# Performance work log

Measured on AMD Instinct MI355X. Metric: run time of the kernel, lower is better.

## Reference

```python
import jax, jax.numpy as jnp
import numpy as np

N = 50000      # nodes
E = 800000     # edges per sampled adjacency
F_IN = 128     # input features
H = 256        # hidden
C = 112        # classes (ogbn-proteins)
L = 8          # num_layers
EPS = 1e-5     # BatchNorm eps


def setup_inputs() -> dict:
    key = jax.random.key(0)
    ks = jax.random.split(key, 8)
    x = jax.random.normal(ks[0], (N, F_IN), dtype=jnp.float32)
    edge1 = jax.random.randint(ks[1], (2, E), 0, N)
    edge2 = jax.random.randint(ks[2], (2, E), 0, N)
    in_W = jax.random.normal(ks[3], (F_IN, H), dtype=jnp.float32) * 0.05
    in_b = jnp.zeros((H,), jnp.float32)
    convW = jax.random.normal(ks[4], (L, H, H), dtype=jnp.float32) * 0.05
    convB = jnp.zeros((L, H), jnp.float32)
    bn_gamma = jnp.ones((L, H), jnp.float32)
    bn_beta = jnp.zeros((L, H), jnp.float32)
    out_W = jax.random.normal(ks[5], (H, C), dtype=jnp.float32) * 0.05
    out_b = jnp.zeros((C,), jnp.float32)
    layer_w = jax.random.normal(ks[6], (L,), dtype=jnp.float32)
    return dict(x=x, edge1=edge1, edge2=edge2, in_W=in_W, in_b=in_b,
                convW=convW, convB=convB, bn_gamma=bn_gamma, bn_beta=bn_beta,
                out_W=out_W, out_b=out_b, layer_w=layer_w)


def _gcn_norm(edge_index):
    # GCNConv default: add self-loops, sym-normalize D^{-1/2} A_hat D^{-1/2}.
    loops = jnp.arange(N)
    row = jnp.concatenate([edge_index[0], loops])  # source
    col = jnp.concatenate([edge_index[1], loops])  # target
    deg = jax.ops.segment_sum(jnp.ones_like(row, jnp.float32), col, num_segments=N)
    dinv = jnp.where(deg > 0, jax.lax.rsqrt(deg), 0.0)
    return row, col, dinv[row] * dinv[col]


def reference(x, edge1, edge2, in_W, in_b, convW, convB, bn_gamma, bn_beta,
              out_W, out_b, layer_w):
    adj1 = _gcn_norm(edge1)
    adj2 = _gcn_norm(edge2)
    h = x @ in_W + in_b                                  # input_fc: [N, H]
    w = jax.nn.softmax(layer_w)                          # residual layer weights
    acc = jnp.zeros_like(h)
    for i in range(L):
        row, col, norm = adj1 if i < L // 2 else adj2
        t = h @ convW[i] + convB[i]                      # GCNConv linear
        msg = t[row] * norm[:, None]                     # gather + scale  [E+N, H]
        h = jax.ops.segment_sum(msg, col, num_segments=N)  # scatter-add SpMM
        mu = h.mean(axis=0)                              # BatchNorm1d (batch stats)
        var = h.var(axis=0)
        h = (h - mu) * jax.lax.rsqrt(var + EPS) * bn_gamma[i] + bn_beta[i]
        h = jax.nn.relu(h)                               # dropout is identity in eval
        acc = acc + w[i] * h                             # weighted residual sum
    out = acc @ out_W + out_b                            # out_fc: [N, C]
    return jax.nn.log_softmax(out, axis=1)
```

## Files before the change

### kernel.cpp

```cpp
#include <hip/hip_runtime.h>
#include <math.h>

#define NN 50000
#define HH 256
#define FIN 128
#define CC 112
#define LL 8
#define EE 800000
#define EPSB 1e-5f
#define NGRP 8
#define NPG (NN / NGRP)
#define SLW 32
#define NSL (HH / SLW)
#define BCAP 110000

typedef unsigned short u16;
typedef unsigned int u32;
typedef __attribute__((ext_vector_type(8))) short bf16x8;
typedef __attribute__((ext_vector_type(4))) float f32x4;

__device__ __forceinline__ u16 f2bf(float f) {
    u32 u = __float_as_uint(f);
    u32 r = (u + 0x7FFFu + ((u >> 16) & 1u)) >> 16;
    return (u16)r;
}
__device__ __forceinline__ float bflo(u32 u) { return __uint_as_float(u << 16); }
__device__ __forceinline__ float bfhi(u32 u) { return __uint_as_float(u & 0xFFFF0000u); }
__device__ __forceinline__ float bf1(u16 u) { return __uint_as_float(((u32)u) << 16); }

__device__ __forceinline__ void gload16(const u16* g, u16* l) {
    __builtin_amdgcn_global_load_lds(
        (const __attribute__((address_space(1))) void*)g,
        (__attribute__((address_space(3))) void*)l, 16, 0, 0);
}

__global__ __launch_bounds__(256) void k_part(const int* __restrict__ ed1,
                                              const int* __restrict__ ed2,
                                              int* __restrict__ bcnt,
                                              u32* __restrict__ bucket) {
    __shared__ int hist[16], base[16], cnt2[16];
    const int t = threadIdx.x;
    if (t < 16) { hist[t] = 0; cnt2[t] = 0; }
    __syncthreads();
    const int e0 = blockIdx.x * 2048;
    int myb[8]; u32 myp[8];
#pragma unroll
    for (int k = 0; k < 8; ++k) {
        int e = e0 + k * 256 + t;
        myb[k] = -1;
        if (e < 2 * EE) {
            const int* ed = (e < EE) ? ed1 : ed2;
            int ee = (e < EE) ? e : e - EE;
            int c = ed[ee + EE];
            int r = ed[ee];
            int b = ((e >= EE) ? 8 : 0) | (c / NPG);
            myb[k] = b;
            myp[k] = ((u32)c << 16) | (u32)r;
            atomicAdd(&hist[b], 1);
        }
    }
    __syncthreads();
    if (t < 16) base[t] = atomicAdd(&bcnt[t], hist[t]);
    __syncthreads();
#pragma unroll
    for (int k = 0; k < 8; ++k) {
        if (myb[k] >= 0) {
            int off = atomicAdd(&cnt2[myb[k]], 1);
            bucket[(size_t)myb[k] * BCAP + base[myb[k]] + off] = myp[k];
        }
    }
}

__global__ __launch_bounds__(256) void k_fillB(const u32* __restrict__ bucket,
                                               const int* __restrict__ bcnt,
                                               int* __restrict__ cur,
                                               u16* __restrict__ src1p,
                                               u16* __restrict__ src2p) {
    const int b = blockIdx.x & 15;
    const int n = bcnt[b];
    u16* sp = (b < 8) ? src1p : src2p;
    int* cu = (b < 8) ? cur : cur + NN;
    const u32* bk = bucket + (size_t)b * BCAP;
    const int stride = (gridDim.x >> 4) * 256;
    for (int i = (blockIdx.x >> 4) * 256 + threadIdx.x; i < n; i += stride) {
        u32 p = bk[i];
        int c = p >> 16;
        int r = p & 0xFFFFu;
        int pos = atomicAdd(&cu[c], 1);
        sp[(c << 6) + pos] = (u16)r;
    }
}

__global__ void k_dinv2(const int* __restrict__ deg, float* __restrict__ dinv1,
                        float* __restrict__ dinv2, int n) {
    int v = blockIdx.x * blockDim.x + threadIdx.x;
    if (v >= 2 * n) return;
    float* d = (v < n) ? dinv1 : dinv2;
    int vv = (v < n) ? v : v - n;
    d[vv] = rsqrtf((float)(deg[v] + 1));
}

__global__ void k_wt(const float* __restrict__ W, u16* __restrict__ Wt, int K, int N) {
    __shared__ u16 sm[32][33];
    const float* Wl = W + (size_t)blockIdx.z * K * N;
    u16* Wtl = Wt + (size_t)blockIdx.z * K * N;
    int k0 = blockIdx.y * 32, n0 = blockIdx.x * 32;
    int tx = threadIdx.x, ty = threadIdx.y;
#pragma unroll
    for (int r = 0; r < 32; r += 8)
        sm[ty + r][tx] = f2bf(Wl[(size_t)(k0 + ty + r) * N + n0 + tx]);
    __syncthreads();
#pragma unroll
    for (int r = 0; r < 32; r += 8)
        Wtl[(size_t)(n0 + ty + r) * K + k0 + tx] = sm[tx][ty + r];
}

__global__ void k_outwt(const float* __restrict__ outW, const float* __restrict__ outb,
                        u16* __restrict__ outWt, float* __restrict__ obb) {
    int idx = blockIdx.x * 256 + threadIdx.x;
    if (idx >= 128 * 256) return;
    int n = idx >> 8, k = idx & 255;
    float v = (n < CC) ? outW[(size_t)k * CC + n] : 0.f;
    outWt[(size_t)n * HH + k] = f2bf(v);
    if (idx < 128) obb[idx] = (idx < CC) ? outb[idx] : 0.f;
}

__global__ void k_xcast(const float* __restrict__ x, u16* __restrict__ xb, int n4) {
    int i = blockIdx.x * blockDim.x + threadIdx.x;
    if (i >= n4) return;
    float4 v = ((const float4*)x)[i];
    ushort4 o;
    o.x = f2bf(v.x); o.y = f2bf(v.y); o.z = f2bf(v.z); o.w = f2bf(v.w);
    *(ushort4*)(xb + ((size_t)i << 2)) = o;
}

template <bool F32OUT, bool SWIZ, bool SLICED>
__global__ __launch_bounds__(256) void k_gemm_bf16(const u16* __restrict__ A,
                                                   const u16* __restrict__ Bt,
                                                   const float* __restrict__ bias,
                                                   const float* __restrict__ rowscale,
                                                   void* __restrict__ Cout,
                                                   int M, int Nc, int K) {
    int m0, n0;
    if (SWIZ) {
        int id = blockIdx.x;
        int g = id >> 4, r = id & 15;
        int m = g * 8 + (r & 7);
        if (m * 128 >= M) return;
        m0 = m * 128;
        n0 = (r >> 3) * 128;
    } else {
        m0 = blockIdx.x * 128;
        n0 = 0;
    }
    __shared__ u16 As[128 * 32];
    __shared__ u16 Bs[128 * 32];
    const int tid = threadIdx.x;
    const int w = tid >> 6, lane = tid & 63;
    const int wr = (w >> 1) * 64, wc = (w & 1) * 64;
    const int lm = lane & 15, lq = lane >> 4;

    f32x4 acc[4][4];
#pragma unroll
    for (int i = 0; i < 4; ++i)
#pragma unroll
        for (int j = 0; j < 4; ++j) acc[i][j] = (f32x4){0.f, 0.f, 0.f, 0.f};

    const int srow = w * 16 + (lane >> 2);
    const int scol = (lane & 3) * 8;

    for (int k0 = 0; k0 < K; k0 += 32) {
        int gm = m0 + srow;        if (gm >= M) gm = M - 1;
        gload16(A + (size_t)gm * K + k0 + scol, As + (size_t)(w * 64) * 8);
        int gm2 = m0 + 64 + srow;  if (gm2 >= M) gm2 = M - 1;
        gload16(A + (size_t)gm2 * K + k0 + scol, As + (size_t)(256 + w * 64) * 8);
        gload16(Bt + (size_t)(n0 + srow) * K + k0 + scol, Bs + (size_t)(w * 64) * 8);
        gload16(Bt + (size_t)(n0 + 64 + srow) * K + k0 + scol, Bs + (size_t)(256 + w * 64) * 8);
        __syncthreads();

        bf16x8 af[4], bfr[4];
#pragma unroll
        for (int i = 0; i < 4; ++i)
            af[i] = *(const bf16x8*)(As + (wr + i * 16 + lm) * 32 + lq * 8);
#pragma unroll
        for (int j = 0; j < 4; ++j)
            bfr[j] = *(const bf16x8*)(Bs + (wc + j * 16 + lm) * 32 + lq * 8);
#pragma unroll
        for (int i = 0; i < 4; ++i)
#pragma unroll
            for (int j = 0; j < 4; ++j)
                acc[i][j] = __builtin_amdgcn_mfma_f32_16x16x32_bf16(af[i], bfr[j], acc[i][j], 0, 0, 0);
        __syncthreads();
    }

#pragma unroll
    for (int j = 0; j < 4; ++j) {
        int gc = n0 + wc + j * 16 + lm;
        float bj = (gc < Nc) ? bias[gc] : 0.f;
#pragma unroll
        for (int i = 0; i < 4; ++i) {
#pragma unroll
            for (int r = 0; r < 4; ++r) {
                int gr = m0 + wr + i * 16 + lq * 4 + r;
                if (gr < M && gc < Nc) {
                    float rs = rowscale ? rowscale[gr] : 1.0f;
                    float val = (acc[i][j][r] + bj) * rs;
                    if (F32OUT)
                        ((float*)Cout)[(size_t)gr * Nc + gc] = val;
                    else if (SLICED)
                        ((u16*)Cout)[((size_t)(gc >> 5) * M + gr) * SLW + (gc & 31)] = f2bf(val);
                    else
                        ((u16*)Cout)[(size_t)gr * Nc + gc] = f2bf(val);
                }
            }
        }
    }
}

__global__ __launch_bounds__(512) void k_spmm_sl8(const u16* __restrict__ ts,
                                                  const int* __restrict__ deg,
                                                  const u16* __restrict__ srcp,
                                                  const float* __restrict__ dinv,
                                                  u16* __restrict__ hpre,
                                                  float* __restrict__ bns,
                                                  float* __restrict__ bnq) {
    __shared__ float lsum[8][SLW];
    __shared__ float lsq[8][SLW];
    const int s = blockIdx.x & 7;
    const int nb = blockIdx.x >> 3;
    const int w = threadIdx.x >> 6;
    const int lane = threadIdx.x & 63;
    const int sub = lane >> 3;
    const int li = lane & 7;
    const u16* tsl = ts + (size_t)s * NN * SLW + li * 4;

    const int v = nb * 64 + w * 8 + sub;
    float4 ssum = make_float4(0.f, 0.f, 0.f, 0.f);
    float4 ssq  = make_float4(0.f, 0.f, 0.f, 0.f);

    if (v < NN) {
        const u16* src = srcp + ((size_t)v << 6);
        const float dv = dinv[v];
        uint2 a = *(const uint2*)(tsl + (size_t)v * SLW);
        float4 A;
        A.x = bflo(a.x); A.y = bfhi(a.x); A.z = bflo(a.y); A.w = bfhi(a.y);
        int end = deg[v];
        int j = 0;
        for (; j + 16 <= end; j += 16) {
            uint4 sp0 = *(const uint4*)(src + j);
            uint4 sp1 = *(const uint4*)(src + j + 8);
            uint2 b0 = *(const uint2*)(tsl + (size_t)(sp0.x & 0xFFFFu) * SLW);
            uint2 b1 = *(const uint2*)(tsl + (size_t)(sp0.x >> 16) * SLW);
            uint2 b2 = *(const uint2*)(tsl + (size_t)(sp0.y & 0xFFFFu) * SLW);
            uint2 b3 = *(const uint2*)(tsl + (size_t)(sp0.y >> 16) * SLW);
            uint2 b4 = *(const uint2*)(tsl + (size_t)(sp0.z & 0xFFFFu) * SLW);
            uint2 b5 = *(const uint2*)(tsl + (size_t)(sp0.z >> 16) * SLW);
            uint2 b6 = *(const uint2*)(tsl + (size_t)(sp0.w & 0xFFFFu) * SLW);
            uint2 b7 = *(const uint2*)(tsl + (size_t)(sp0.w >> 16) * SLW);
            uint2 c0 = *(const uint2*)(tsl + (size_t)(sp1.x & 0xFFFFu) * SLW);
            uint2 c1 = *(const uint2*)(tsl + (size_t)(sp1.x >> 16) * SLW);
            uint2 c2 = *(const uint2*)(tsl + (size_t)(sp1.y & 0xFFFFu) * SLW);
            uint2 c3 = *(const uint2*)(tsl + (size_t)(sp1.y >> 16) * SLW);
            uint2 c4 = *(const uint2*)(tsl + (size_t)(sp1.z & 0xFFFFu) * SLW);
            uint2 c5 = *(const uint2*)(tsl + (size_t)(sp1.z >> 16) * SLW);
            uint2 c6 = *(const uint2*)(tsl + (size_t)(sp1.w & 0xFFFFu) * SLW);
            uint2 c7 = *(const uint2*)(tsl + (size_t)(sp1.w >> 16) * SLW);
            A.x += bflo(b0.x) + bflo(b1.x) + bflo(b2.x) + bflo(b3.x)
                 + bflo(b4.x) + bflo(b5.x) + bflo(b6.x) + bflo(b7.x)
                 + bflo(c0.x) + bflo(c1.x) + bflo(c2.x) + bflo(c3.x)
                 + bflo(c4.x) + bflo(c5.x) + bflo(c6.x) + bflo(c7.x);
            A.y += bfhi(b0.x) + bfhi(b1.x) + bfhi(b2.x) + bfhi(b3.x)
                 + bfhi(b4.x) + bfhi(b5.x) + bfhi(b6.x) + bfhi(b7.x)
                 + bfhi(c0.x) + bfhi(c1.x) + bfhi(c2.x) + bfhi(c3.x)
                 + bfhi(c4.x) + bfhi(c5.x) + bfhi(c6.x) + bfhi(c7.x);
            A.z += bflo(b0.y) + bflo(b1.y) + bflo(b2.y) + bflo(b3.y)
                 + bflo(b4.y) + bflo(b5.y) + bflo(b6.y) + bflo(b7.y)
                 + bflo(c0.y) + bflo(c1.y) + bflo(c2.y) + bflo(c3.y)
                 + bflo(c4.y) + bflo(c5.y) + bflo(c6.y) + bflo(c7.y);
            A.w += bfhi(b0.y) + bfhi(b1.y) + bfhi(b2.y) + bfhi(b3.y)
                 + bfhi(b4.y) + bfhi(b5.y) + bfhi(b6.y) + bfhi(b7.y)
                 + bfhi(c0.y) + bfhi(c1.y) + bfhi(c2.y) + bfhi(c3.y)
                 + bfhi(c4.y) + bfhi(c5.y) + bfhi(c6.y) + bfhi(c7.y);
        }
        for (; j + 8 <= end; j += 8) {
            uint4 sp = *(const uint4*)(src + j);
            uint2 b0 = *(const uint2*)(tsl + (size_t)(sp.x & 0xFFFFu) * SLW);
            uint2 b1 = *(const uint2*)(tsl + (size_t)(sp.x >> 16) * SLW);
            uint2 b2 = *(const uint2*)(tsl + (size_t)(sp.y & 0xFFFFu) * SLW);
            uint2 b3 = *(const uint2*)(tsl + (size_t)(sp.y >> 16) * SLW);
            uint2 b4 = *(const uint2*)(tsl + (size_t)(sp.z & 0xFFFFu) * SLW);
            uint2 b5 = *(const uint2*)(tsl + (size_t)(sp.z >> 16) * SLW);
            uint2 b6 = *(const uint2*)(tsl + (size_t)(sp.w & 0xFFFFu) * SLW);
            uint2 b7 = *(const uint2*)(tsl + (size_t)(sp.w >> 16) * SLW);
            A.x += bflo(b0.x) + bflo(b1.x) + bflo(b2.x) + bflo(b3.x)
                 + bflo(b4.x) + bflo(b5.x) + bflo(b6.x) + bflo(b7.x);
            A.y += bfhi(b0.x) + bfhi(b1.x) + bfhi(b2.x) + bfhi(b3.x)
                 + bfhi(b4.x) + bfhi(b5.x) + bfhi(b6.x) + bfhi(b7.x);
            A.z += bflo(b0.y) + bflo(b1.y) + bflo(b2.y) + bflo(b3.y)
                 + bflo(b4.y) + bflo(b5.y) + bflo(b6.y) + bflo(b7.y);
            A.w += bfhi(b0.y) + bfhi(b1.y) + bfhi(b2.y) + bfhi(b3.y)
                 + bfhi(b4.y) + bfhi(b5.y) + bfhi(b6.y) + bfhi(b7.y);
        }
        for (; j + 2 <= end; j += 2) {
            int s0 = src[j], s1 = src[j + 1];
            uint2 b0 = *(const uint2*)(tsl + (size_t)s0 * SLW);
            uint2 b1 = *(const uint2*)(tsl + (size_t)s1 * SLW);
            A.x += bflo(b0.x) + bflo(b1.x);
            A.y += bfhi(b0.x) + bfhi(b1.x);
            A.z += bflo(b0.y) + bflo(b1.y);
            A.w += bfhi(b0.y) + bfhi(b1.y);
        }
        if (j < end) {
            uint2 b0 = *(const uint2*)(tsl + (size_t)src[j] * SLW);
            A.x += bflo(b0.x); A.y += bfhi(b0.x);
            A.z += bflo(b0.y); A.w += bfhi(b0.y);
        }
        ushort4 o;
        o.x = f2bf(A.x * dv); o.y = f2bf(A.y * dv);
        o.z = f2bf(A.z * dv); o.w = f2bf(A.w * dv);
        *(ushort4*)(hpre + (size_t)v * HH + s * SLW + li * 4) = o;
        float fx = bf1(o.x), fy = bf1(o.y), fz = bf1(o.z), fw = bf1(o.w);
        ssum.x = fx; ssum.y = fy; ssum.z = fz; ssum.w = fw;
        ssq.x = fx * fx; ssq.y = fy * fy; ssq.z = fz * fz; ssq.w = fw * fw;
    }

#pragma unroll
    for (int d = 8; d < 64; d <<= 1) {
        ssum.x += __shfl_xor(ssum.x, d, 64);
        ssum.y += __shfl_xor(ssum.y, d, 64);
        ssum.z += __shfl_xor(ssum.z, d, 64);
        ssum.w += __shfl_xor(ssum.w, d, 64);
        ssq.x += __shfl_xor(ssq.x, d, 64);
        ssq.y += __shfl_xor(ssq.y, d, 64);
        ssq.z += __shfl_xor(ssq.z, d, 64);
        ssq.w += __shfl_xor(ssq.w, d, 64);
    }
    if (lane < 8) {
        *(float4*)&lsum[w][lane * 4] = ssum;
        *(float4*)&lsq[w][lane * 4] = ssq;
    }
    __syncthreads();
    int t = threadIdx.x;
    if (t < SLW) {
        float a = 0.f;
#pragma unroll
        for (int ww = 0; ww < 8; ++ww) a += lsum[ww][t];
        atomicAdd(&bns[(nb & 7) * HH + s * SLW + t], a);
    } else if (t < 2 * SLW) {
        int c = t - SLW;
        float a = 0.f;
#pragma unroll
        for (int ww = 0; ww < 8; ++ww) a += lsq[ww][c];
        atomicAdd(&bnq[(nb & 7) * HH + s * SLW + c], a);
    }
}

__global__ __launch_bounds__(256) void k_bnnorm(const u16* __restrict__ hpre,
                         u16* __restrict__ accb, u16* __restrict__ hb,
                         const float* __restrict__ bins,
                         const float* __restrict__ gamma, const float* __restrict__ beta,
                         const float* __restrict__ wArr, int layer) {
    __shared__ float sscale[HH], sshift[HH];
    const float invN = 1.0f / (float)NN;
    {
        int tcol = threadIdx.x;
        float m = 0.f, qq = 0.f;
#pragma unroll
        for (int b = 0; b < 8; ++b) {
            m += bins[b * HH + tcol];
            qq += bins[(8 + b) * HH + tcol];
        }
        m *= invN;
        float var = qq * invN - m * m;
        float sc = rsqrtf(var + EPSB) * gamma[tcol];
        sscale[tcol] = sc;
        sshift[tcol] = beta[tcol] - m * sc;
    }
    __syncthreads();
    int idx = blockIdx.x * blockDim.x + threadIdx.x;
    if (idx >= NN * (HH / 4)) return;
    int c = (idx & 63) << 2;
    float w = wArr[layer];
    ushort4 hv = ((const ushort4*)hpre)[idx];
    ushort4 av = ((const ushort4*)accb)[idx];
    u16* hp = &hv.x;
    u16* ap = &av.x;
    ushort4 oh, oa;
    u16* ohp = &oh.x;
    u16* oap = &oa.x;
#pragma unroll
    for (int k = 0; k < 4; ++k) {
        float v = fmaf(bf1(hp[k]), sscale[c + k], sshift[c + k]);
        v = fmaxf(v, 0.f);
        oap[k] = f2bf(fmaf(w, v, bf1(ap[k])));
        ohp[k] = f2bf(v);
    }
    ((ushort4*)accb)[idx] = oa;
    *(ushort4*)(hb + ((size_t)idx << 2)) = oh;
}

__global__ void k_softmaxw(const float* __restrict__ lw, float* __restrict__ wArr) {
    if (threadIdx.x == 0 && blockIdx.x == 0) {
        float m = -3.0e38f;
        for (int i = 0; i < LL; ++i) m = fmaxf(m, lw[i]);
        float e[LL]; float sum = 0.f;
        for (int i = 0; i < LL; ++i) { e[i] = expf(lw[i] - m); sum += e[i]; }
        for (int i = 0; i < LL; ++i) wArr[i] = e[i] / sum;
    }
}

__global__ __launch_bounds__(256) void k_logsoftmax(const float* __restrict__ z,
                                                    float* __restrict__ out) {
    int gt = blockIdx.x * blockDim.x + threadIdx.x;
    int v = gt >> 6;
    int lane = threadIdx.x & 63;
    if (v >= NN) return;
    const float* row = z + (size_t)v * CC;
    float v0 = row[lane];
    float v1 = (lane + 64 < CC) ? row[lane + 64] : -3.0e38f;
    float m = fmaxf(v0, v1);
#pragma unroll
    for (int d = 1; d < 64; d <<= 1) m = fmaxf(m, __shfl_xor(m, d, 64));
    float e = expf(v0 - m) + ((lane + 64 < CC) ? expf(v1 - m) : 0.f);
#pragma unroll
    for (int d = 1; d < 64; d <<= 1) e += __shfl_xor(e, d, 64);
    float lse = m + logf(e);
    out[(size_t)v * CC + lane] = v0 - lse;
    if (lane + 64 < CC) out[(size_t)v * CC + lane + 64] = v1 - lse;
}

extern "C" void kernel_launch(void* const* d_in, const int* in_sizes, int n_in,
                              void* d_out, int out_size, void* d_ws, size_t ws_size,
                              hipStream_t stream) {
    const float* x     = (const float*)d_in[0];
    const int*   e1    = (const int*)d_in[1];
    const int*   e2    = (const int*)d_in[2];
    const float* inW   = (const float*)d_in[3];
    const float* inb   = (const float*)d_in[4];
    const float* convW = (const float*)d_in[5];
    const float* convB = (const float*)d_in[6];
    const float* gamma = (const float*)d_in[7];
    const float* beta  = (const float*)d_in[8];
    const float* outW  = (const float*)d_in[9];
    const float* outb  = (const float*)d_in[10];
    const float* lw    = (const float*)d_in[11];

    char* ws = (char*)d_ws;
    size_t off = 0;
    auto alloc = [&](size_t bytes) -> void* {
        void* p = ws + off;
        off = (off + bytes + 255) & ~(size_t)255;
        return p;
    };
    u16*   hb    = (u16*)alloc((size_t)NN * HH * 2);
    u16*   tb    = (u16*)alloc((size_t)NN * HH * 2);
    u16*   hpre  = (u16*)alloc((size_t)NN * HH * 2);
    u16*   accb  = (u16*)alloc((size_t)NN * HH * 2);
    u16*   convWt= (u16*)alloc((size_t)LL * HH * HH * 2);
    u16*   inWt  = (u16*)alloc((size_t)HH * FIN * 2);
    u16*   outWt = (u16*)alloc((size_t)128 * HH * 2);
    float* obb   = (float*)alloc(128 * 4);
    float* dinv1 = (float*)alloc((size_t)NN * 4);
    float* dinv2 = (float*)alloc((size_t)NN * 4);
    u16*   src1p = (u16*)alloc((size_t)NN * 64 * 2);
    u16*   src2p = (u16*)alloc((size_t)NN * 64 * 2);
    int*   curz  = (int*)alloc((size_t)2 * NN * 4);
    float* bnsq  = (float*)alloc((size_t)LL * 16 * HH * 4);
    float* wArr  = (float*)alloc(64);
    u32*   bucket= (u32*)alloc((size_t)16 * BCAP * 4);
    int*   bcnt  = (int*)alloc(16 * 4);
    u16*   xb    = tb;
    float* logits = (float*)hpre;

    int* cur1 = curz;

    hipMemsetAsync(curz, 0, (size_t)2 * NN * 4, stream);
    hipMemsetAsync(bnsq, 0, (size_t)LL * 16 * HH * 4, stream);
    hipMemsetAsync(accb, 0, (size_t)NN * HH * 2, stream);
    hipMemsetAsync(bcnt, 0, 16 * 4, stream);

    k_part<<<(2 * EE + 2047) / 2048, 256, 0, stream>>>(e1, e2, bcnt, bucket);
    k_fillB<<<16 * 64, 256, 0, stream>>>(bucket, bcnt, curz, src1p, src2p);
    k_dinv2<<<(2 * NN + 255) / 256, 256, 0, stream>>>(curz, dinv1, dinv2, NN);

    k_softmaxw<<<1, 64, 0, stream>>>(lw, wArr);

    {
        dim3 g(HH / 32, HH / 32, LL);
        dim3 b(32, 8);
        k_wt<<<g, b, 0, stream>>>(convW, convWt, HH, HH);
        dim3 g2(HH / 32, FIN / 32, 1);
        k_wt<<<g2, b, 0, stream>>>(inW, inWt, FIN, HH);
        k_outwt<<<128, 256, 0, stream>>>(outW, outb, outWt, obb);
    }
    k_xcast<<<(NN * FIN / 4 + 255) / 256, 256, 0, stream>>>(x, xb, NN * FIN / 4);

    const int MT = (NN + 127) / 128;
    const int GSW = ((MT + 7) / 8) * 16;
    k_gemm_bf16<false, true, false><<<GSW, 256, 0, stream>>>(xb, inWt, inb, nullptr, hb,
                                                             NN, HH, FIN);

    const int NBL = (NN + 63) / 64;
    const int SPB = NBL * NSL;
    const int ELB = (NN * (HH / 4) + 255) / 256;
    for (int i = 0; i < LL; ++i) {
        const int* dg = (i < LL / 2) ? cur1 : (curz + NN);
        const u16* sr = (i < LL / 2) ? src1p : src2p;
        const float* dv = (i < LL / 2) ? dinv1 : dinv2;
        float* bins = bnsq + (size_t)i * 16 * HH;
        k_gemm_bf16<false, true, true><<<GSW, 256, 0, stream>>>(hb,
                                                          convWt + (size_t)i * HH * HH,
                                                          convB + (size_t)i * HH, dv, tb,
                                                          NN, HH, HH);
        k_spmm_sl8<<<SPB, 512, 0, stream>>>(tb, dg, sr, dv, hpre, bins, bins + 8 * HH);
        k_bnnorm<<<ELB, 256, 0, stream>>>(hpre, accb, hb, bins,
                                          gamma + (size_t)i * HH, beta + (size_t)i * HH,
                                          wArr, i);
    }

    k_gemm_bf16<true, false, false><<<MT, 256, 0, stream>>>(accb, outWt, obb, nullptr, logits,
                                                            NN, CC, HH);
    k_logsoftmax<<<NN / 4, 256, 0, stream>>>(logits, (float*)d_out);
}
```

Baseline: 1.185 ms.

## Sort SpMM destination nodes by degree to balance per-wave work

```diff
diff --git a/kernel.cpp b/kernel.cpp
--- a/kernel.cpp
+++ b/kernel.cpp
@@ -92,12 +92,34 @@
 }
 
 __global__ void k_dinv2(const int* __restrict__ deg, float* __restrict__ dinv1,
-                        float* __restrict__ dinv2, int n) {
+                        float* __restrict__ dinv2, int* __restrict__ hist, int n) {
     int v = blockIdx.x * blockDim.x + threadIdx.x;
     if (v >= 2 * n) return;
     float* d = (v < n) ? dinv1 : dinv2;
     int vv = (v < n) ? v : v - n;
-    d[vv] = rsqrtf((float)(deg[v] + 1));
+    int dg = deg[v];
+    d[vv] = rsqrtf((float)(dg + 1));
+    int bin = dg > 63 ? 63 : dg;
+    atomicAdd(&hist[((v >= n) ? 64 : 0) + bin], 1);
+}
+
+__global__ void k_dscan(const int* __restrict__ hist, int* __restrict__ off) {
+    int g = threadIdx.x;
+    if (g >= 2) return;
+    int s = 0;
+    for (int d = 0; d < 64; ++d) { off[g * 64 + d] = s; s += hist[g * 64 + d]; }
+}
+
+__global__ void k_dplace(const int* __restrict__ deg, int* __restrict__ off,
+                         u16* __restrict__ perm1, u16* __restrict__ perm2, int n) {
+    int v = blockIdx.x * blockDim.x + threadIdx.x;
+    if (v >= 2 * n) return;
+    int g = (v >= n) ? 1 : 0;
+    int vv = g ? v - n : v;
+    int dg = deg[v];
+    int bin = dg > 63 ? 63 : dg;
+    int pos = atomicAdd(&off[g * 64 + bin], 1);
+    (g ? perm2 : perm1)[pos] = (u16)vv;
 }
 
 __global__ void k_wt(const float* __restrict__ W, u16* __restrict__ Wt, int K, int N) {
@@ -221,6 +243,7 @@
                                                   const int* __restrict__ deg,
                                                   const u16* __restrict__ srcp,
                                                   const float* __restrict__ dinv,
+                                                  const u16* __restrict__ perm,
                                                   u16* __restrict__ hpre,
                                                   float* __restrict__ bns,
                                                   float* __restrict__ bnq) {
@@ -234,11 +257,12 @@
     const int li = lane & 7;
     const u16* tsl = ts + (size_t)s * NN * SLW + li * 4;
 
-    const int v = nb * 64 + w * 8 + sub;
+    const int vi = nb * 64 + w * 8 + sub;
     float4 ssum = make_float4(0.f, 0.f, 0.f, 0.f);
     float4 ssq  = make_float4(0.f, 0.f, 0.f, 0.f);
 
-    if (v < NN) {
+    if (vi < NN) {
+        const int v = perm[vi];
         const u16* src = srcp + ((size_t)v << 6);
         const float dv = dinv[v];
         uint2 a = *(const uint2*)(tsl + (size_t)v * SLW);
@@ -469,6 +493,10 @@
     float* wArr  = (float*)alloc(64);
     u32*   bucket= (u32*)alloc((size_t)16 * BCAP * 4);
     int*   bcnt  = (int*)alloc(16 * 4);
+    u16*   perm1 = (u16*)alloc((size_t)NN * 2);
+    u16*   perm2 = (u16*)alloc((size_t)NN * 2);
+    int*   dhist = (int*)alloc(128 * 4);
+    int*   doff  = (int*)alloc(128 * 4);
     u16*   xb    = tb;
     float* logits = (float*)hpre;
 
@@ -478,10 +506,13 @@
     hipMemsetAsync(bnsq, 0, (size_t)LL * 16 * HH * 4, stream);
     hipMemsetAsync(accb, 0, (size_t)NN * HH * 2, stream);
     hipMemsetAsync(bcnt, 0, 16 * 4, stream);
+    hipMemsetAsync(dhist, 0, 128 * 4, stream);
 
     k_part<<<(2 * EE + 2047) / 2048, 256, 0, stream>>>(e1, e2, bcnt, bucket);
     k_fillB<<<16 * 64, 256, 0, stream>>>(bucket, bcnt, curz, src1p, src2p);
-    k_dinv2<<<(2 * NN + 255) / 256, 256, 0, stream>>>(curz, dinv1, dinv2, NN);
+    k_dinv2<<<(2 * NN + 255) / 256, 256, 0, stream>>>(curz, dinv1, dinv2, dhist, NN);
+    k_dscan<<<1, 64, 0, stream>>>(dhist, doff);
+    k_dplace<<<(2 * NN + 255) / 256, 256, 0, stream>>>(curz, doff, perm1, perm2, NN);
 
     k_softmaxw<<<1, 64, 0, stream>>>(lw, wArr);
 
@@ -507,12 +538,13 @@
         const int* dg = (i < LL / 2) ? cur1 : (curz + NN);
         const u16* sr = (i < LL / 2) ? src1p : src2p;
         const float* dv = (i < LL / 2) ? dinv1 : dinv2;
+        const u16* pm = (i < LL / 2) ? perm1 : perm2;
         float* bins = bnsq + (size_t)i * 16 * HH;
         k_gemm_bf16<false, true, true><<<GSW, 256, 0, stream>>>(hb,
                                                           convWt + (size_t)i * HH * HH,
                                                           convB + (size_t)i * HH, dv, tb,
                                                           NN, HH, HH);
-        k_spmm_sl8<<<SPB, 512, 0, stream>>>(tb, dg, sr, dv, hpre, bins, bins + 8 * HH);
+        k_spmm_sl8<<<SPB, 512, 0, stream>>>(tb, dg, sr, dv, pm, hpre, bins, bins + 8 * HH);
         k_bnnorm<<<ELB, 256, 0, stream>>>(hpre, accb, hb, bins,
                                           gamma + (size_t)i * HH, beta + (size_t)i * HH,
                                           wArr, i);
```

Result: slower. 1.484 ms (+25.2%).
